# Optimization experiments

Hardware: AMD Instinct MI355X
Metric: run time of the kernel (lower is better)

## Reference

```python
import jax, jax.numpy as jnp
import numpy as np
import math

NUM_HEADS = 8

def setup_inputs() -> dict:
    key = jax.random.key(0)
    ks = jax.random.split(key, 5)
    b, h, w, c = 4, 128, 128, 256
    x = jax.random.normal(ks[0], (b, h, w, c), dtype=jnp.float32)
    scale = 1.0 / math.sqrt(c)  # keep weights reasonably scaled (kaiming-like)
    Wq = jax.random.normal(ks[1], (c, c), dtype=jnp.float32) * scale
    Wk = jax.random.normal(ks[2], (c, c), dtype=jnp.float32) * scale
    Wv = jax.random.normal(ks[3], (c, c), dtype=jnp.float32) * scale
    Wout = jax.random.normal(ks[4], (c, c), dtype=jnp.float32) * scale
    return {"x": x, "Wq": Wq, "Wk": Wk, "Wv": Wv, "Wout": Wout}

def reference(x, Wq, Wk, Wv, Wout):
    b, h, w, c = x.shape
    hw = h * w
    heads = NUM_HEADS
    dh = c // heads
    xs = x.reshape(b, hw, c)
    q = xs @ Wq  # (b, hw, c)
    k = xs @ Wk
    v = xs @ Wv

    def split_heads(t):
        # (b, hw, c) -> (b, c, hw) -> (b, heads, dh, hw)
        return t.transpose(0, 2, 1).reshape(b, heads, dh, hw)

    q = split_heads(q)
    k = split_heads(k)
    v = split_heads(v)
    # L2-normalize along the feature (hw) axis; original has no epsilon
    q = q / jnp.linalg.norm(q, axis=-1, keepdims=True)
    k = k / jnp.linalg.norm(k, axis=-1, keepdims=True)
    d_k = q.shape[-1]  # = hw
    attn = jnp.einsum('bhcd,bhed->bhce', q, k) / math.sqrt(d_k)  # (b,heads,dh,dh)
    attn = jax.nn.softmax(attn, axis=-1)
    vals = jnp.einsum('bhce,bhed->bhcd', attn, v)  # (b,heads,dh,hw)
    vals = vals.transpose(0, 3, 1, 2).reshape(b, hw, c)
    out = (vals @ Wout).reshape(b, h, w, c)
    return out
```

## Files before the change

kernel.cpp:

```cpp
#include <hip/hip_runtime.h>


#define B_   4
#define HW_  16384
#define C_   256

typedef __attribute__((ext_vector_type(8))) short short8;
typedef __attribute__((ext_vector_type(4))) float floatx4;

__device__ __forceinline__ unsigned short f2bf(float f) {
  unsigned u = __builtin_bit_cast(unsigned, f);
  u += 0x7FFFu + ((u >> 16) & 1u);
  return (unsigned short)(u >> 16);
}

__device__ __forceinline__ void gl_lds16(const unsigned short* g, unsigned short* l) {
  __builtin_amdgcn_global_load_lds(
      (const __attribute__((address_space(1))) unsigned int*)g,
      (__attribute__((address_space(3))) unsigned int*)l, 16, 0, 0);
}

__global__ __launch_bounds__(512) void k_sgemm(const float* __restrict__ x,
                                               float* __restrict__ part) {
  __shared__ unsigned short Pt[256 * 128];
  int bid = blockIdx.x;
  int hs = bid & 1, ks = (bid >> 1) & 31, b = bid >> 6;
  const float* xv = x + ((size_t)(b * HW_ + ks * 512)) * C_;
  int t = threadIdx.x, lane = t & 63, w = t >> 6;
  int rw = w >> 2, cw = w & 3;
  int m0 = hs * 128 + rw * 64;
  int n0 = cw * 64;
  int l15 = lane & 15, l4 = lane >> 4;
  int s_cq  = (lane >> 3) | (w << 3);
  int s_hpl = lane & 7;
  floatx4 acc[4][4];
  floatx4 z = {0.f, 0.f, 0.f, 0.f};
#pragma unroll
  for (int i = 0; i < 4; i++)
#pragma unroll
    for (int j = 0; j < 4; j++) acc[i][j] = z;

#pragma unroll
  for (int e = 0; e < 8; e++) {
    int hp = s_hpl | (e << 3);
    const float* src = xv + ((size_t)(hp * 2)) * C_ + s_cq * 4;
    float4 v0 = *(const float4*)src;
    float4 v1 = *(const float4*)(src + C_);
    float a0[4] = {v0.x, v0.y, v0.z, v0.w};
    float a1[4] = {v1.x, v1.y, v1.z, v1.w};
#pragma unroll
    for (int i = 0; i < 4; i++) {
      unsigned u = (unsigned)f2bf(a0[i]) | ((unsigned)f2bf(a1[i]) << 16);
      int r = s_cq * 4 + i;
      int slot = (hp >> 2) ^ (r & 15);
      ((unsigned*)Pt)[r * 64 + slot * 4 + (hp & 3)] = u;
    }
  }
  __syncthreads();

  float4 pA[8], pB[8];
  for (int ph = 0; ph < 4; ph++) {
    if (ph < 3) {
#pragma unroll
      for (int e = 0; e < 8; e++) {
        int hp = s_hpl | (e << 3);
        const float* src = xv + ((size_t)((ph + 1) * 128 + hp * 2)) * C_ + s_cq * 4;
        pA[e] = *(const float4*)src;
        pB[e] = *(const float4*)(src + C_);
      }
    }
#pragma unroll
    for (int kk = 0; kk < 4; kk++) {
      short8 af[4], bfv[4];
      int oct = kk * 4 + l4;
#pragma unroll
      for (int tm = 0; tm < 4; tm++) {
        int row = m0 + tm * 16 + l15;
        af[tm] = *(const short8*)(Pt + row * 128 + ((oct ^ (row & 15)) * 8));
      }
#pragma unroll
      for (int tn = 0; tn < 4; tn++) {
        int row = n0 + tn * 16 + l15;
        bfv[tn] = *(const short8*)(Pt + row * 128 + ((oct ^ (row & 15)) * 8));
      }
#pragma unroll
      for (int tm = 0; tm < 4; tm++)
#pragma unroll
        for (int tn = 0; tn < 4; tn++)
          acc[tm][tn] = __builtin_amdgcn_mfma_f32_16x16x32_bf16(af[tm], bfv[tn],
                                                                acc[tm][tn], 0, 0, 0);
    }
    if (ph < 3) {
      __syncthreads();
#pragma unroll
      for (int e = 0; e < 8; e++) {
        int hp = s_hpl | (e << 3);
        float a0[4] = {pA[e].x, pA[e].y, pA[e].z, pA[e].w};
        float a1[4] = {pB[e].x, pB[e].y, pB[e].z, pB[e].w};
#pragma unroll
        for (int i = 0; i < 4; i++) {
          unsigned u = (unsigned)f2bf(a0[i]) | ((unsigned)f2bf(a1[i]) << 16);
          int r = s_cq * 4 + i;
          int slot = (hp >> 2) ^ (r & 15);
          ((unsigned*)Pt)[r * 64 + slot * 4 + (hp & 3)] = u;
        }
      }
      __syncthreads();
    }
  }
  float* pb = part + (size_t)(b * 32 + ks) * 65536;
#pragma unroll
  for (int tm = 0; tm < 4; tm++)
#pragma unroll
    for (int tn = 0; tn < 4; tn++)
#pragma unroll
      for (int r = 0; r < 4; r++) {
        int m = m0 + tm * 16 + l4 * 4 + r;
        int n = n0 + tn * 16 + l15;
        pb[m * 256 + n] = acc[tm][tn][r];
      }
}

__global__ __launch_bounds__(256) void k_sred(const float* __restrict__ part,
                                              float* __restrict__ S) {
  int g = blockIdx.x * 256 + threadIdx.x;
  int b = g >> 14, off = (g & 16383) * 4;
  const float* p = part + ((size_t)b << 21) + off;
  float4 s = {0.f, 0.f, 0.f, 0.f};
#pragma unroll
  for (int k = 0; k < 32; k++) {
    float4 v = *(const float4*)(p + ((size_t)k << 16));
    s.x += v.x; s.y += v.y; s.z += v.z; s.w += v.w;
  }
  *(float4*)(S + ((size_t)b << 16) + off) = s;
}

__global__ __launch_bounds__(256) void k_gemm_sw(const float* __restrict__ S,
                                                 const float* __restrict__ Wq,
                                                 const float* __restrict__ Wk,
                                                 float* __restrict__ SWq,
                                                 float* __restrict__ SWk) {
  __shared__ float Ast[16][68];
  __shared__ float Bs[16][68];
  int bid = blockIdx.x;
  int nt = bid & 7, mt = (bid >> 3) & 3, b = bid >> 5;
  int mb = mt * 64;
  const float* Wsel = (nt < 4) ? Wq : Wk;
  int nb = (nt & 3) * 64;
  int t = threadIdx.x, tx = t & 15, ty = t >> 4;
  float acc[4][4] = {};
  for (int kt = 0; kt < 16; kt++) {
    {
      int row = t >> 2, kq = t & 3;
      float4 v = *(const float4*)(S + ((size_t)(b * C_ + mb + row)) * C_ + kt * 16 + kq * 4);
      Ast[kq * 4 + 0][row] = v.x; Ast[kq * 4 + 1][row] = v.y;
      Ast[kq * 4 + 2][row] = v.z; Ast[kq * 4 + 3][row] = v.w;
    }
    {
      int kk = t >> 4, n4 = t & 15;
      float4 v = *(const float4*)(Wsel + ((size_t)(kt * 16 + kk)) * C_ + nb + n4 * 4);
      *(float4*)&Bs[kk][n4 * 4] = v;
    }
    __syncthreads();
#pragma unroll
    for (int k = 0; k < 16; k++) {
      float4 a4 = *(const float4*)&Ast[k][ty * 4];
      float4 b4 = *(const float4*)&Bs[k][tx * 4];
      float a[4] = {a4.x, a4.y, a4.z, a4.w};
      float bb[4] = {b4.x, b4.y, b4.z, b4.w};
#pragma unroll
      for (int i = 0; i < 4; i++)
#pragma unroll
        for (int j = 0; j < 4; j++) acc[i][j] += a[i] * bb[j];
    }
    __syncthreads();
  }
#pragma unroll
  for (int i = 0; i < 4; i++)
#pragma unroll
    for (int j = 0; j < 4; j++) {
      int row = mb + ty * 4 + i;
      int ng = nt * 64 + tx * 4 + j;
      if (ng < 256) SWq[((size_t)(b * C_ + row)) * C_ + ng] = acc[i][j];
      else          SWk[((size_t)(b * C_ + row)) * C_ + ng - 256] = acc[i][j];
    }
}

__global__ __launch_bounds__(256) void k_fuse(const float* __restrict__ Wq,
                                              const float* __restrict__ Wk,
                                              const float* __restrict__ SWq,
                                              const float* __restrict__ SWk,
                                              const float* __restrict__ Wout,
                                              float* __restrict__ U) {
  __shared__ float Wqh[256][32];
  __shared__ float Wkh[256][32];
  __shared__ float SWqh[256][32];
  __shared__ float SWkh[256][32];
  __shared__ float Lg[32][33];
  __shared__ float qp[8][32], kp[8][32], qin[32], kin[32];
  int b = blockIdx.x >> 3, h = blockIdx.x & 7;
  int t = threadIdx.x;
  int col = t & 31, rgrp = t >> 5;
  for (int r0 = 0; r0 < 256; r0 += 8) {
    int row = r0 + rgrp;
    Wqh[row][col]  = Wq[(size_t)row * C_ + h * 32 + col];
    Wkh[row][col]  = Wk[(size_t)row * C_ + h * 32 + col];
    SWqh[row][col] = SWq[((size_t)(b * C_ + row)) * C_ + h * 32 + col];
    SWkh[row][col] = SWk[((size_t)(b * C_ + row)) * C_ + h * 32 + col];
  }
  __syncthreads();
  {
    float g[4] = {0.f, 0.f, 0.f, 0.f};
    for (int k = 0; k < 256; k++) {
      float swk = SWkh[k][col];
#pragma unroll
      for (int r = 0; r < 4; r++) g[r] += Wqh[k][rgrp + 8 * r] * swk;
    }
#pragma unroll
    for (int r = 0; r < 4; r++) Lg[rgrp + 8 * r][col] = g[r];
  }
  {
    float sq = 0.f, sk = 0.f;
    for (int k = rgrp * 32; k < rgrp * 32 + 32; k++) {
      sq += Wqh[k][col] * SWqh[k][col];
      sk += Wkh[k][col] * SWkh[k][col];
    }
    qp[rgrp][col] = sq;
    kp[rgrp][col] = sk;
  }
  __syncthreads();
  if (t < 32) {
    float a = 0.f;
#pragma unroll
    for (int p = 0; p < 8; p++) a += qp[p][t];
    qin[t] = rsqrtf(a);
  } else if (t < 64) {
    int j = t - 32;
    float a = 0.f;
#pragma unroll
    for (int p = 0; p < 8; p++) a += kp[p][j];
    kin[j] = rsqrtf(a);
  }
  __syncthreads();
  if (t < 32) {
    float row[32];
    float mx = -1e30f;
#pragma unroll
    for (int j = 0; j < 32; j++) {
      row[j] = Lg[t][j] * qin[t] * kin[j] * 0.0078125f;
      mx = fmaxf(mx, row[j]);
    }
    float sum = 0.f;
#pragma unroll
    for (int j = 0; j < 32; j++) { row[j] = __expf(row[j] - mx); sum += row[j]; }
    float inv = 1.0f / sum;
#pragma unroll
    for (int j = 0; j < 32; j++) Lg[t][j] = row[j] * inv;
  }
  __syncthreads();
  float (*Wo)[256] = reinterpret_cast<float(*)[256]>(&Wqh[0][0]);
#pragma unroll
  for (int r = 0; r < 32; r++) Wo[r][t] = Wout[((size_t)(h * 32 + r)) * C_ + t];
  __syncthreads();
  for (int j = 0; j < 32; j++) {
    float a = 0.f;
#pragma unroll
    for (int i2 = 0; i2 < 32; i2++) a += Lg[i2][j] * Wo[i2][t];
    U[((size_t)(b * C_ + h * 32 + j)) * C_ + t] = a;
  }
}

__global__ __launch_bounds__(256) void k_gemm_w3(const float* __restrict__ Wv,
                                                 const float* __restrict__ U,
                                                 unsigned short* __restrict__ W3bT) {
  __shared__ float Ast[16][68];
  __shared__ float Bs[16][68];
  int bid = blockIdx.x;
  int nt = bid & 3, mt = (bid >> 2) & 3, b = bid >> 4;
  int mb = mt * 64, nb = nt * 64;
  int t = threadIdx.x, tx = t & 15, ty = t >> 4;
  float acc[4][4] = {};
  for (int kt = 0; kt < 16; kt++) {
    {
      int row = t >> 2, kq = t & 3;
      float4 v = *(const float4*)(Wv + ((size_t)(mb + row)) * C_ + kt * 16 + kq * 4);
      Ast[kq * 4 + 0][row] = v.x; Ast[kq * 4 + 1][row] = v.y;
      Ast[kq * 4 + 2][row] = v.z; Ast[kq * 4 + 3][row] = v.w;
    }
    {
      int kk = t >> 4, n4 = t & 15;
      float4 v = *(const float4*)(U + ((size_t)(b * C_ + kt * 16 + kk)) * C_ + nb + n4 * 4);
      *(float4*)&Bs[kk][n4 * 4] = v;
    }
    __syncthreads();
#pragma unroll
    for (int k = 0; k < 16; k++) {
      float4 a4 = *(const float4*)&Ast[k][ty * 4];
      float4 b4 = *(const float4*)&Bs[k][tx * 4];
      float a[4] = {a4.x, a4.y, a4.z, a4.w};
      float bb[4] = {b4.x, b4.y, b4.z, b4.w};
#pragma unroll
      for (int i = 0; i < 4; i++)
#pragma unroll
        for (int j = 0; j < 4; j++) acc[i][j] += a[i] * bb[j];
    }
    __syncthreads();
  }
#pragma unroll
  for (int i = 0; i < 4; i++)
#pragma unroll
    for (int j = 0; j < 4; j++)
      W3bT[((size_t)(b * C_ + nb + tx * 4 + j)) * C_ + mb + ty * 4 + i] = f2bf(acc[i][j]);
}

__global__ __launch_bounds__(256) void k_out(const float* __restrict__ x,
                                             const unsigned short* __restrict__ W3bT,
                                             float* __restrict__ out) {
  __shared__ unsigned short Bt[256 * 64];
  int mtile = blockIdx.x;
  int b = mtile >> 7;
  const float* Ax = x + (size_t)mtile * 128 * C_;
  const unsigned short* Bb = W3bT + (size_t)b * C_ * C_;
  int t = threadIdx.x, lane = t & 63, w = t >> 6;
  int hf = w >> 1, c2 = w & 1;
  int l8 = lane >> 3, l7 = lane & 7;
  int srcoct = l7 ^ l8;
  int l15 = lane & 15, l4 = lane >> 4;
  floatx4 acc[4][8];
  floatx4 z = {0.f, 0.f, 0.f, 0.f};
#pragma unroll
  for (int i = 0; i < 4; i++)
#pragma unroll
    for (int j = 0; j < 8; j++) acc[i][j] = z;
  for (int s = 0; s < 4; s++) {
    if (s) __syncthreads();
#pragma unroll
    for (int i = 0; i < 8; i++) {
      int ib = w * 8 + i;
      int row = ib * 8 + l8;
      gl_lds16(Bb + (size_t)row * C_ + s * 64 + srcoct * 8, Bt + ib * 512);
    }
    __syncthreads();
#pragma unroll
    for (int kk = 0; kk < 2; kk++) {
      short8 af[4], bfv[8];
      int oct = kk * 4 + l4;
#pragma unroll
      for (int tm = 0; tm < 4; tm++) {
        int row = hf * 64 + tm * 16 + l15;
        const float* p = Ax + (size_t)row * C_ + s * 64 + oct * 8;
        float4 u0 = *(const float4*)p;
        float4 u1 = *(const float4*)(p + 4);
        short8 v;
        v[0] = (short)f2bf(u0.x); v[1] = (short)f2bf(u0.y);
        v[2] = (short)f2bf(u0.z); v[3] = (short)f2bf(u0.w);
        v[4] = (short)f2bf(u1.x); v[5] = (short)f2bf(u1.y);
        v[6] = (short)f2bf(u1.z); v[7] = (short)f2bf(u1.w);
        af[tm] = v;
      }
#pragma unroll
      for (int tn = 0; tn < 8; tn++) {
        int row = c2 * 128 + tn * 16 + l15;
        bfv[tn] = *(const short8*)(Bt + row * 64 + ((oct ^ (row & 7)) * 8));
      }
#pragma unroll
      for (int tm = 0; tm < 4; tm++)
#pragma unroll
        for (int tn = 0; tn < 8; tn++)
          acc[tm][tn] = __builtin_amdgcn_mfma_f32_16x16x32_bf16(af[tm], bfv[tn],
                                                                acc[tm][tn], 0, 0, 0);
    }
  }
  float* ob = out + (size_t)mtile * 128 * C_;
#pragma unroll
  for (int tm = 0; tm < 4; tm++)
#pragma unroll
    for (int tn = 0; tn < 8; tn++)
#pragma unroll
      for (int r = 0; r < 4; r++) {
        int m = hf * 64 + tm * 16 + l4 * 4 + r;
        int n = c2 * 128 + tn * 16 + l15;
        ob[(size_t)m * C_ + n] = acc[tm][tn][r];
      }
}

extern "C" void kernel_launch(void* const* d_in, const int* in_sizes, int n_in,
                              void* d_out, int out_size, void* d_ws, size_t ws_size,
                              hipStream_t stream) {
  const float* x    = (const float*)d_in[0];
  const float* Wq   = (const float*)d_in[1];
  const float* Wk   = (const float*)d_in[2];
  const float* Wv   = (const float*)d_in[3];
  const float* Wout = (const float*)d_in[4];
  float* out = (float*)d_out;

  float* part = (float*)d_ws;
  float* S    = part + (size_t)8388608;
  float* SWq  = S + 262144;
  float* SWk  = SWq + 262144;
  float* U    = SWk + 262144;
  unsigned short* W3bT = (unsigned short*)(U + 262144);

  k_sgemm<<<dim3(256), dim3(512), 0, stream>>>(x, part);
  k_sred<<<dim3(256), dim3(256), 0, stream>>>(part, S);
  k_gemm_sw<<<dim3(128), dim3(256), 0, stream>>>(S, Wq, Wk, SWq, SWk);
  k_fuse<<<dim3(32), dim3(256), 0, stream>>>(Wq, Wk, SWq, SWk, Wout, U);
  k_gemm_w3<<<dim3(64), dim3(256), 0, stream>>>(Wv, U, W3bT);
  k_out<<<dim3(512), dim3(256), 0, stream>>>(x, W3bT, out);
}
```

Measured before the change: 219.9 us.

## Emit bf16 copy of x in first pass and stage it via LDS in output GEMM

The first Gram-matrix kernel now also writes a bf16 copy of x to workspace (from one of the two half-blocks), and the final output GEMM reads that bf16 copy through direct global-to-LDS loads instead of re-reading fp32 x and converting per fragment. This halves the bytes the output kernel reads for x and removes redundant conversions, at the cost of an extra 32 MB write in the first kernel. The f2bf helper is also switched to the compiler's native bf16 conversion.

After: 224.4 us. 2.0% more time.

```diff
diff --git a/kernel.cpp b/kernel.cpp
--- a/kernel.cpp
+++ b/kernel.cpp
@@ -9,9 +9,7 @@
 typedef __attribute__((ext_vector_type(4))) float floatx4;
 
 __device__ __forceinline__ unsigned short f2bf(float f) {
-  unsigned u = __builtin_bit_cast(unsigned, f);
-  u += 0x7FFFu + ((u >> 16) & 1u);
-  return (unsigned short)(u >> 16);
+  return __builtin_bit_cast(unsigned short, (__bf16)f);
 }
 
 __device__ __forceinline__ void gl_lds16(const unsigned short* g, unsigned short* l) {
@@ -21,11 +19,13 @@
 }
 
 __global__ __launch_bounds__(512) void k_sgemm(const float* __restrict__ x,
-                                               float* __restrict__ part) {
+                                               float* __restrict__ part,
+                                               unsigned short* __restrict__ xb) {
   __shared__ unsigned short Pt[256 * 128];
   int bid = blockIdx.x;
   int hs = bid & 1, ks = (bid >> 1) & 31, b = bid >> 6;
   const float* xv = x + ((size_t)(b * HW_ + ks * 512)) * C_;
+  unsigned short* xbp = xb + ((size_t)(b * HW_ + ks * 512)) * C_;
   int t = threadIdx.x, lane = t & 63, w = t >> 6;
   int rw = w >> 2, cw = w & 3;
   int m0 = hs * 128 + rw * 64;
@@ -48,6 +48,13 @@
     float4 v1 = *(const float4*)(src + C_);
     float a0[4] = {v0.x, v0.y, v0.z, v0.w};
     float a1[4] = {v1.x, v1.y, v1.z, v1.w};
+    if (hs == 0) {
+      ushort4 h0, h1;
+      h0.x = f2bf(a0[0]); h0.y = f2bf(a0[1]); h0.z = f2bf(a0[2]); h0.w = f2bf(a0[3]);
+      h1.x = f2bf(a1[0]); h1.y = f2bf(a1[1]); h1.z = f2bf(a1[2]); h1.w = f2bf(a1[3]);
+      *(ushort4*)(xbp + (size_t)(hp * 2) * C_ + s_cq * 4) = h0;
+      *(ushort4*)(xbp + (size_t)(hp * 2 + 1) * C_ + s_cq * 4) = h1;
+    }
 #pragma unroll
     for (int i = 0; i < 4; i++) {
       unsigned u = (unsigned)f2bf(a0[i]) | ((unsigned)f2bf(a1[i]) << 16);
@@ -97,6 +104,13 @@
         int hp = s_hpl | (e << 3);
         float a0[4] = {pA[e].x, pA[e].y, pA[e].z, pA[e].w};
         float a1[4] = {pB[e].x, pB[e].y, pB[e].z, pB[e].w};
+        if (hs == 0) {
+          ushort4 h0, h1;
+          h0.x = f2bf(a0[0]); h0.y = f2bf(a0[1]); h0.z = f2bf(a0[2]); h0.w = f2bf(a0[3]);
+          h1.x = f2bf(a1[0]); h1.y = f2bf(a1[1]); h1.z = f2bf(a1[2]); h1.w = f2bf(a1[3]);
+          *(ushort4*)(xbp + (size_t)((ph + 1) * 128 + hp * 2) * C_ + s_cq * 4) = h0;
+          *(ushort4*)(xbp + (size_t)((ph + 1) * 128 + hp * 2 + 1) * C_ + s_cq * 4) = h1;
+        }
 #pragma unroll
         for (int i = 0; i < 4; i++) {
           unsigned u = (unsigned)f2bf(a0[i]) | ((unsigned)f2bf(a1[i]) << 16);
@@ -313,13 +327,14 @@
       W3bT[((size_t)(b * C_ + nb + tx * 4 + j)) * C_ + mb + ty * 4 + i] = f2bf(acc[i][j]);
 }
 
-__global__ __launch_bounds__(256) void k_out(const float* __restrict__ x,
+__global__ __launch_bounds__(256) void k_out(const unsigned short* __restrict__ xb,
                                              const unsigned short* __restrict__ W3bT,
                                              float* __restrict__ out) {
+  __shared__ unsigned short At[128 * 64];
   __shared__ unsigned short Bt[256 * 64];
   int mtile = blockIdx.x;
   int b = mtile >> 7;
-  const float* Ax = x + (size_t)mtile * 128 * C_;
+  const unsigned short* Ab = xb + (size_t)mtile * 128 * C_;
   const unsigned short* Bb = W3bT + (size_t)b * C_ * C_;
   int t = threadIdx.x, lane = t & 63, w = t >> 6;
   int hf = w >> 1, c2 = w & 1;
@@ -335,6 +350,12 @@
   for (int s = 0; s < 4; s++) {
     if (s) __syncthreads();
 #pragma unroll
+    for (int i = 0; i < 4; i++) {
+      int ia = w * 4 + i;
+      int row = ia * 8 + l8;
+      gl_lds16(Ab + (size_t)row * C_ + s * 64 + srcoct * 8, At + ia * 512);
+    }
+#pragma unroll
     for (int i = 0; i < 8; i++) {
       int ib = w * 8 + i;
       int row = ib * 8 + l8;
@@ -348,15 +369,7 @@
 #pragma unroll
       for (int tm = 0; tm < 4; tm++) {
         int row = hf * 64 + tm * 16 + l15;
-        const float* p = Ax + (size_t)row * C_ + s * 64 + oct * 8;
-        float4 u0 = *(const float4*)p;
-        float4 u1 = *(const float4*)(p + 4);
-        short8 v;
-        v[0] = (short)f2bf(u0.x); v[1] = (short)f2bf(u0.y);
-        v[2] = (short)f2bf(u0.z); v[3] = (short)f2bf(u0.w);
-        v[4] = (short)f2bf(u1.x); v[5] = (short)f2bf(u1.y);
-        v[6] = (short)f2bf(u1.z); v[7] = (short)f2bf(u1.w);
-        af[tm] = v;
+        af[tm] = *(const short8*)(At + row * 64 + ((oct ^ (row & 7)) * 8));
       }
 #pragma unroll
       for (int tn = 0; tn < 8; tn++) {
@@ -400,11 +413,12 @@
   float* SWk  = SWq + 262144;
   float* U    = SWk + 262144;
   unsigned short* W3bT = (unsigned short*)(U + 262144);
-
-  k_sgemm<<<dim3(256), dim3(512), 0, stream>>>(x, part);
+  unsigned short* xb   = W3bT + (size_t)262144;
+
+  k_sgemm<<<dim3(256), dim3(512), 0, stream>>>(x, part, xb);
   k_sred<<<dim3(256), dim3(256), 0, stream>>>(part, S);
   k_gemm_sw<<<dim3(128), dim3(256), 0, stream>>>(S, Wq, Wk, SWq, SWk);
   k_fuse<<<dim3(32), dim3(256), 0, stream>>>(Wq, Wk, SWq, SWk, Wout, U);
   k_gemm_w3<<<dim3(64), dim3(256), 0, stream>>>(Wv, U, W3bT);
-  k_out<<<dim3(512), dim3(256), 0, stream>>>(x, W3bT, out);
-}
+  k_out<<<dim3(512), dim3(256), 0, stream>>>(xb, W3bT, out);
+}
```

## Stage k_out A tiles in LDS via async loads, use hardware bf16 convert, remap k_sgemm blocks

Applied to the files above, without the earlier changes.

k_out now copies the fp32 activation tile into a swizzled LDS buffer with global_load_lds instead of each wave reading global memory directly. This gives coalesced loads and overlaps them with the B tile staging. The f2bf helper now uses the compiler's __bf16 conversion so the hardware convert instruction can replace the manual rounding. k_sgemm's block-index mapping is reordered so the two half-blocks that share an x chunk are spaced apart in launch order. The extra 32KB of LDS per block may lower k_out occupancy.

Result: no change. 219.2 us (-0.3%).

```diff
diff --git a/kernel.cpp b/kernel.cpp
--- a/kernel.cpp
+++ b/kernel.cpp
@@ -9,9 +9,7 @@
 typedef __attribute__((ext_vector_type(4))) float floatx4;
 
 __device__ __forceinline__ unsigned short f2bf(float f) {
-  unsigned u = __builtin_bit_cast(unsigned, f);
-  u += 0x7FFFu + ((u >> 16) & 1u);
-  return (unsigned short)(u >> 16);
+  return __builtin_bit_cast(unsigned short, (__bf16)f);
 }
 
 __device__ __forceinline__ void gl_lds16(const unsigned short* g, unsigned short* l) {
@@ -20,11 +18,19 @@
       (__attribute__((address_space(3))) unsigned int*)l, 16, 0, 0);
 }
 
+__device__ __forceinline__ void gl_lds16f(const float* g, float* l) {
+  __builtin_amdgcn_global_load_lds(
+      (const __attribute__((address_space(1))) unsigned int*)g,
+      (__attribute__((address_space(3))) unsigned int*)l, 16, 0, 0);
+}
+
 __global__ __launch_bounds__(512) void k_sgemm(const float* __restrict__ x,
                                                float* __restrict__ part) {
   __shared__ unsigned short Pt[256 * 128];
   int bid = blockIdx.x;
-  int hs = bid & 1, ks = (bid >> 1) & 31, b = bid >> 6;
+  int chunkid = (bid & 7) | ((bid >> 4) << 3);
+  int hs = (bid >> 3) & 1;
+  int ks = chunkid & 31, b = chunkid >> 5;
   const float* xv = x + ((size_t)(b * HW_ + ks * 512)) * C_;
   int t = threadIdx.x, lane = t & 63, w = t >> 6;
   int rw = w >> 2, cw = w & 3;
@@ -316,6 +322,7 @@
 __global__ __launch_bounds__(256) void k_out(const float* __restrict__ x,
                                              const unsigned short* __restrict__ W3bT,
                                              float* __restrict__ out) {
+  __shared__ float Atf[128 * 64];
   __shared__ unsigned short Bt[256 * 64];
   int mtile = blockIdx.x;
   int b = mtile >> 7;
@@ -326,6 +333,8 @@
   int l8 = lane >> 3, l7 = lane & 7;
   int srcoct = l7 ^ l8;
   int l15 = lane & 15, l4 = lane >> 4;
+  int ar_l = lane >> 4;
+  int aslot = lane & 15;
   floatx4 acc[4][8];
   floatx4 z = {0.f, 0.f, 0.f, 0.f};
 #pragma unroll
@@ -334,6 +343,13 @@
     for (int j = 0; j < 8; j++) acc[i][j] = z;
   for (int s = 0; s < 4; s++) {
     if (s) __syncthreads();
+#pragma unroll
+    for (int i = 0; i < 8; i++) {
+      int j = w * 8 + i;
+      int row = j * 4 + ar_l;
+      int usrc = aslot ^ (row & 15);
+      gl_lds16f(Ax + (size_t)row * C_ + s * 64 + usrc * 4, Atf + j * 256);
+    }
 #pragma unroll
     for (int i = 0; i < 8; i++) {
       int ib = w * 8 + i;
@@ -348,14 +364,15 @@
 #pragma unroll
       for (int tm = 0; tm < 4; tm++) {
         int row = hf * 64 + tm * 16 + l15;
-        const float* p = Ax + (size_t)row * C_ + s * 64 + oct * 8;
-        float4 u0 = *(const float4*)p;
-        float4 u1 = *(const float4*)(p + 4);
+        int u0 = (oct * 2) ^ (row & 15);
+        int u1 = (oct * 2 + 1) ^ (row & 15);
+        float4 f0 = *(const float4*)(Atf + row * 64 + u0 * 4);
+        float4 f1 = *(const float4*)(Atf + row * 64 + u1 * 4);
         short8 v;
-        v[0] = (short)f2bf(u0.x); v[1] = (short)f2bf(u0.y);
-        v[2] = (short)f2bf(u0.z); v[3] = (short)f2bf(u0.w);
-        v[4] = (short)f2bf(u1.x); v[5] = (short)f2bf(u1.y);
-        v[6] = (short)f2bf(u1.z); v[7] = (short)f2bf(u1.w);
+        v[0] = (short)f2bf(f0.x); v[1] = (short)f2bf(f0.y);
+        v[2] = (short)f2bf(f0.z); v[3] = (short)f2bf(f0.w);
+        v[4] = (short)f2bf(f1.x); v[5] = (short)f2bf(f1.y);
+        v[6] = (short)f2bf(f1.z); v[7] = (short)f2bf(f1.w);
         af[tm] = v;
       }
 #pragma unroll
```
